# Performance work log

Hardware: AMD Instinct MI355X
Metric: run time of the kernel (lower is better)

## Reference

```python
import jax, jax.numpy as jnp
import numpy as np
from jax import lax

BOS, EOS = 1, 2
MAX_LEN = 16
BEAM = 4
VOCAB = 32000
INF = 1e9


def _gather_beams(x, idx):
    # x: [B, K, ...] or [B, K]; idx: [B, k]
    if x.ndim == 3:
        return jnp.take_along_axis(x, idx[:, :, None], axis=1)
    return jnp.take_along_axis(x, idx, axis=1)


def setup_inputs() -> dict:
    key = jax.random.key(0)
    k1, k2, k3, k4 = jax.random.split(key, 4)
    B, S, D = 16, 128, 512
    return {
        "src_input": jax.random.randint(k1, (B, S), 0, VOCAB),
        "E_src": jax.random.normal(k2, (VOCAB, D), jnp.float32) * 0.02,
        "E_tgt": jax.random.normal(k3, (VOCAB, D), jnp.float32) * 0.02,
        "W": jax.random.normal(k4, (D, VOCAB), jnp.float32) * 0.02,
        "b": jnp.zeros((VOCAB,), jnp.float32),
    }


def _beam_search(src_input, E_src, E_tgt, W, b):
    B = src_input.shape[0]
    # tile_by_beam: repeat each batch row beam_size times
    src = jnp.repeat(src_input, BEAM, axis=0)                     # [B*BEAM, S]
    # stub encoder: embedding + masked mean pool (pad token = 0)
    enc = E_src[src]                                              # [B*BEAM, S, D]
    keep = (src != 0).astype(enc.dtype)[..., None]
    pooled = (enc * keep).sum(1) / jnp.maximum(keep.sum(1), 1.0)  # [B*BEAM, D]

    alive_seq = jnp.zeros((B, BEAM, MAX_LEN), jnp.int32).at[:, :, 0].set(BOS)
    alive_lp = jnp.full((B, BEAM), -jnp.inf, jnp.float32).at[:, 0].set(0.0)
    fin_seq = jnp.zeros((B, BEAM, MAX_LEN), jnp.int32)
    fin_scores = jnp.full((B, BEAM), -INF, jnp.float32)
    fin_flags = jnp.zeros((B, BEAM), bool)
    batch_fin = jnp.zeros((B,), bool)
    batch_idx = jnp.arange(B)[:, None]

    for t in range(MAX_LEN - 1):
        # stub decoder: last-token embedding + encoder summary -> vocab logits
        last = alive_seq[:, :, t].reshape(B * BEAM)
        logits = (E_tgt[last] + pooled) @ W + b                   # [B*BEAM, V]
        lp = jax.nn.log_softmax(logits, axis=-1).reshape(B, BEAM, VOCAB)
        log_probs = alive_lp[:, :, None] + lp                     # [B, BEAM, V]
        lpen = jnp.float32(t + 1)
        flat = (log_probs / lpen).reshape(B, BEAM * VOCAB)
        topk_scores, topk_ids = lax.top_k(flat, BEAM * 2)         # [B, 2*BEAM]
        topk_lp = topk_scores * lpen
        if t == 0:
            beam_idx = jnp.tile(jnp.arange(BEAM), (B, 2))
        else:
            beam_idx = topk_ids // VOCAB
        tok = topk_ids % VOCAB
        topk_seq = alive_seq[batch_idx, beam_idx]                 # [B, 2*BEAM, L]
        topk_seq = topk_seq.at[:, :, t + 1].set(tok.astype(jnp.int32))
        topk_fin = tok == EOS
        # alive set: penalize finished candidates
        curr = topk_scores + topk_fin.astype(jnp.float32) * -INF
        _, a_idx = lax.top_k(curr, BEAM)
        alive_seq = _gather_beams(topk_seq, a_idx)
        alive_lp = _gather_beams(topk_lp, a_idx)
        # finished set: penalize unfinished + already-finished batches
        fs = (topk_scores + (1.0 - topk_fin.astype(jnp.float32)) * -INF
              + batch_fin[:, None].astype(jnp.float32) * -INF)
        cand_seq = jnp.concatenate([fin_seq, topk_seq], axis=1)   # [B, 3*BEAM, L]
        cand_sc = jnp.concatenate([fin_scores, fs], axis=1)
        cand_fl = jnp.concatenate([fin_flags, topk_fin], axis=1)
        _, f_idx = lax.top_k(cand_sc, BEAM)
        fin_seq = _gather_beams(cand_seq, f_idx)
        fin_scores = _gather_beams(cand_sc, f_idx)
        fin_flags = _gather_beams(cand_fl, f_idx)
        # batch-finished lower-bound test
        lb_alive = alive_lp[:, 0] / lpen
        lowest_fin = jnp.min(fin_scores * fin_flags.astype(jnp.float32), axis=1)
        lowest_fin = lowest_fin + (1.0 - jnp.all(fin_flags, axis=1).astype(jnp.float32)) * -INF
        batch_fin = batch_fin | (lowest_fin >= lb_alive)
    return fin_seq, fin_scores


def reference(src_input, E_src, E_tgt, W, b):
    fin_seq, _ = _beam_search(src_input, E_src, E_tgt, W, b)
    return fin_seq[:, 0]  # one_best_output [B, MAX_LEN] int32
```

## Files before the change

### kernel.cpp

```cpp
#include <hip/hip_runtime.h>
#include <math.h>

#define BATCH 16
#define SRCLEN 128
#define DIM 512
#define VOCABSZ 32000
#define BEAM 4
#define MAXLEN 16
#define NROWS (BATCH*BEAM)
#define BOS_TOK 1
#define EOS_TOK 2
#define NEGINF 1e9f
#define CHUNKS 8
#define CHUNK 4000
#define PCH 8
#define PCL (SRCLEN/PCH)

__global__ __launch_bounds__(512) void k_pool2(const int* __restrict__ src,
                                               const float* __restrict__ Esrc,
                                               float* __restrict__ pp, float* __restrict__ pcnt) {
    int b = blockIdx.x, c = blockIdx.y;
    int d = threadIdx.x;
    float acc = 0.f, cnt = 0.f;
#pragma unroll
    for (int s = 0; s < PCL; ++s) {
        int tok = src[b * SRCLEN + c * PCL + s];
        if (tok != 0) { acc += Esrc[(size_t)tok * DIM + d]; cnt += 1.f; }
    }
    pp[(b * PCH + c) * DIM + d] = acc;
    if (d == 0) pcnt[b * PCH + c] = cnt;
}

__global__ __launch_bounds__(512) void k_poolred(const float* __restrict__ pp,
                                                 const float* __restrict__ pcnt,
                                                 float* __restrict__ pooled) {
    int b = blockIdx.x;
    int d = threadIdx.x;
    float acc = 0.f, cnt = 0.f;
#pragma unroll
    for (int c = 0; c < PCH; ++c) { acc += pp[(b * PCH + c) * DIM + d]; cnt += pcnt[b * PCH + c]; }
    pooled[b * DIM + d] = acc / fmaxf(cnt, 1.f);
}

__global__ __launch_bounds__(1024) void k_init(int* __restrict__ alive_seq, float* __restrict__ alive_lp,
                                               int* __restrict__ fin_seq, float* __restrict__ fin_scores,
                                               int* __restrict__ fin_flags, int* __restrict__ batch_fin) {
    int tid = threadIdx.x;
    alive_seq[tid] = (tid % MAXLEN == 0) ? BOS_TOK : 0;
    fin_seq[tid] = 0;
    if (tid < NROWS) {
        alive_lp[tid] = (tid % BEAM == 0) ? 0.f : -INFINITY;
        fin_scores[tid] = -NEGINF;
        fin_flags[tid] = 0;
    }
    if (tid < BATCH) batch_fin[tid] = 0;
}

__global__ __launch_bounds__(512) void k_x(const float* __restrict__ Etgt,
                                           const float* __restrict__ pooled,
                                           const int* __restrict__ alive_seq, int t,
                                           float* __restrict__ xT) {
    int i = blockIdx.x;
    int d = threadIdx.x;
    int last = alive_seq[i * MAXLEN + t];
    float v = Etgt[(size_t)last * DIM + d] + pooled[(i >> 2) * DIM + d];
    xT[d * NROWS + i] = v;
}

template<int DLEN>
__global__ __launch_bounds__(256) void k_gemm4(const float* __restrict__ xT,
                                               const float* __restrict__ W,
                                               float* __restrict__ partial) {
    int v  = blockIdx.x * 64 + (threadIdx.x & 63);
    int rq = __builtin_amdgcn_readfirstlane(threadIdx.x >> 6);
    int r0 = rq * 16;
    int z  = blockIdx.z;
    int d0 = z * DLEN;
    float acc[16];
#pragma unroll
    for (int i = 0; i < 16; ++i) acc[i] = 0.f;
    const float* wp = W + (size_t)d0 * VOCABSZ + v;
    const float* xp = xT + (size_t)d0 * NROWS + r0;
    for (int dd = 0; dd < DLEN; dd += 4) {
        float w0 = wp[0];
        float w1 = wp[(size_t)VOCABSZ];
        float w2 = wp[(size_t)2 * VOCABSZ];
        float w3 = wp[(size_t)3 * VOCABSZ];
        wp += (size_t)4 * VOCABSZ;
        const float* x0 = xp;
        const float* x1 = xp + NROWS;
        const float* x2 = xp + 2 * NROWS;
        const float* x3 = xp + 3 * NROWS;
        xp += 4 * NROWS;
#pragma unroll
        for (int i = 0; i < 16; ++i) acc[i] = fmaf(x0[i], w0, acc[i]);
#pragma unroll
        for (int i = 0; i < 16; ++i) acc[i] = fmaf(x1[i], w1, acc[i]);
#pragma unroll
        for (int i = 0; i < 16; ++i) acc[i] = fmaf(x2[i], w2, acc[i]);
#pragma unroll
        for (int i = 0; i < 16; ++i) acc[i] = fmaf(x3[i], w3, acc[i]);
    }
    float* op = partial + (size_t)z * NROWS * VOCABSZ + (size_t)r0 * VOCABSZ + v;
#pragma unroll
    for (int i = 0; i < 16; ++i) op[(size_t)i * VOCABSZ] = acc[i];
}

template<int NZ>
__global__ __launch_bounds__(256) void k_part(const float* __restrict__ partial,
                                              const float* __restrict__ bias,
                                              float* __restrict__ pm, float* __restrict__ ps,
                                              float* __restrict__ ptopv, int* __restrict__ ptopi) {
    int row = blockIdx.x, ch = blockIdx.y;
    int tid = threadIdx.x;
    const size_t slab = (size_t)NROWS * VOCABSZ;
    const float4* lr4[NZ];
#pragma unroll
    for (int zz = 0; zz < NZ; ++zz)
        lr4[zz] = (const float4*)(partial + slab * zz + (size_t)row * VOCABSZ + ch * CHUNK);
    const float4* b4 = (const float4*)(bias + ch * CHUNK);

    float va[16]; int np = 0;
    float lv[8]; int li[8];
#pragma unroll
    for (int j = 0; j < 8; ++j) { lv[j] = -INFINITY; li[j] = 0x7FFFFFFF; }

#pragma unroll
    for (int j = 0; j < 4; ++j) {
        int idx = j * 256 + tid;
        if (idx < CHUNK / 4) {
            float4 q = lr4[0][idx];
#pragma unroll
            for (int zz = 1; zz < NZ; ++zz) {
                float4 q2 = lr4[zz][idx];
                q.x += q2.x; q.y += q2.y; q.z += q2.z; q.w += q2.w;
            }
            float4 bb = b4[idx];
            q.x += bb.x; q.y += bb.y; q.z += bb.z; q.w += bb.w;
            int gi = ch * CHUNK + idx * 4;
            float vals[4] = {q.x, q.y, q.z, q.w};
#pragma unroll
            for (int c = 0; c < 4; ++c) {
                float x = vals[c];
                va[np++] = x;
                int v = gi + c;
                if (x > lv[7] || (x == lv[7] && v < li[7])) {
                    lv[7] = x; li[7] = v;
#pragma unroll
                    for (int q2 = 7; q2 > 0; --q2) {
                        bool sw = (lv[q2] > lv[q2-1]) || (lv[q2] == lv[q2-1] && li[q2] < li[q2-1]);
                        if (sw) { float tv = lv[q2]; lv[q2] = lv[q2-1]; lv[q2-1] = tv;
                                  int  ti = li[q2]; li[q2] = li[q2-1]; li[q2-1] = ti; }
                    }
                }
            }
        }
    }

    __shared__ float sred[256];
    float m_t = -INFINITY;
    for (int j = 0; j < np; ++j) m_t = fmaxf(m_t, va[j]);
    sred[tid] = m_t;
    __syncthreads();
    for (int s = 128; s > 0; s >>= 1) { if (tid < s) sred[tid] = fmaxf(sred[tid], sred[tid+s]); __syncthreads(); }
    float m = sred[0];
    __syncthreads();

    float se = 0.f;
    for (int j = 0; j < np; ++j) se += expf(va[j] - m);
    sred[tid] = se;
    __syncthreads();
    for (int s = 128; s > 0; s >>= 1) { if (tid < s) sred[tid] += sred[tid+s]; __syncthreads(); }
    if (tid == 0) { pm[row * CHUNKS + ch] = m; ps[row * CHUNKS + ch] = sred[0]; }

    __shared__ unsigned long long skey[256];
    int pos = 0;
    float* otv = ptopv + ((size_t)row * CHUNKS + ch) * 8;
    int*   oti = ptopi + ((size_t)row * CHUNKS + ch) * 8;
    for (int r = 0; r < 8; ++r) {
        unsigned long long mykey = 0ULL;
        if (pos < 8) {
            unsigned int fb = __float_as_uint(lv[pos]);
            fb = fb ^ ((fb >> 31) ? 0xFFFFFFFFu : 0x80000000u);
            mykey = ((unsigned long long)fb << 32) | (unsigned long long)(0xFFFFFFFFu - (unsigned int)li[pos]);
        }
        skey[tid] = mykey;
        __syncthreads();
        for (int s = 128; s > 0; s >>= 1) { if (tid < s) skey[tid] = (skey[tid] > skey[tid+s]) ? skey[tid] : skey[tid+s]; __syncthreads(); }
        unsigned long long best = skey[0];
        __syncthreads();
        if (mykey == best && mykey != 0ULL) {
            otv[r] = lv[pos];
            oti[r] = li[pos];
            pos++;
        }
        __syncthreads();
    }
}

__device__ inline unsigned long long packkey(float v, int idx) {
    unsigned int fb = __float_as_uint(v);
    fb = fb ^ ((fb >> 31) ? 0xFFFFFFFFu : 0x80000000u);
    return ((unsigned long long)fb << 32) | (unsigned long long)(0xFFFFFFFFu - (unsigned int)idx);
}
__device__ inline float unpack_val(unsigned long long k) {
    unsigned int fb = (unsigned int)(k >> 32);
    fb = fb ^ ((fb >> 31) ? 0x80000000u : 0xFFFFFFFFu);
    return __uint_as_float(fb);
}
__device__ inline int unpack_id(unsigned long long k) {
    return (int)(0xFFFFFFFFu - (unsigned int)(k & 0xFFFFFFFFu));
}
__device__ inline unsigned long long shflxor64(unsigned long long x, int mask) {
    unsigned int lo = (unsigned int)x, hi = (unsigned int)(x >> 32);
    lo = (unsigned int)__shfl_xor((int)lo, mask, 64);
    hi = (unsigned int)__shfl_xor((int)hi, mask, 64);
    return ((unsigned long long)hi << 32) | (unsigned long long)lo;
}
__device__ inline unsigned long long wavemax64(unsigned long long k) {
#pragma unroll
    for (int off = 1; off < 64; off <<= 1) {
        unsigned long long o = shflxor64(k, off);
        k = (o > k) ? o : k;
    }
    return k;
}

__global__ __launch_bounds__(64) void k_mergesel(const float* __restrict__ pm, const float* __restrict__ ps,
                                                 const float* __restrict__ ptopv, const int* __restrict__ ptopi,
                                                 int* __restrict__ alive_seq, float* __restrict__ alive_lp,
                                                 int* __restrict__ fin_seq, float* __restrict__ fin_scores,
                                                 int* __restrict__ fin_flags, int* __restrict__ batch_fin, int t) {
    int b = blockIdx.x;
    int tid = threadIdx.x;
    __shared__ int aseq_old[BEAM][MAXLEN]; __shared__ int fseq_old[BEAM][MAXLEN];
    __shared__ float s_tlp[8]; __shared__ int s_ttok[8], s_tbeam[8];
    __shared__ int s_aidx[4], s_fidx[4];
    __shared__ float s_nfsc[4]; __shared__ int s_nffl[4];
    float lpen = (float)(t + 1);

    { int k = tid >> 4, p = tid & 15;
      aseq_old[k][p] = alive_seq[(b * BEAM + k) * MAXLEN + p];
      fseq_old[k][p] = fin_seq[(b * BEAM + k) * MAXLEN + p]; }

    float rv[4]; int ri[4];
#pragma unroll
    for (int k = 0; k < 4; ++k) {
        rv[k] = ptopv[(size_t)(b * BEAM + k) * 64 + tid];
        ri[k] = ptopi[(size_t)(b * BEAM + k) * 64 + tid];
    }

    float alp[4], fsc[4]; int ffl[4];
#pragma unroll
    for (int k = 0; k < 4; ++k) {
        alp[k] = alive_lp[b * BEAM + k];
        fsc[k] = fin_scores[b * BEAM + k];
        ffl[k] = fin_flags[b * BEAM + k];
    }
    int bf_old = batch_fin[b];

    float srm[4], srl[4];
#pragma unroll
    for (int k = 0; k < 4; ++k) {
        float m = -INFINITY;
#pragma unroll
        for (int c = 0; c < CHUNKS; ++c) m = fmaxf(m, pm[(b * BEAM + k) * CHUNKS + c]);
        float s = 0.f;
#pragma unroll
        for (int c = 0; c < CHUNKS; ++c) s += ps[(b * BEAM + k) * CHUNKS + c] * expf(pm[(b * BEAM + k) * CHUNKS + c] - m);
        srm[k] = m; srl[k] = logf(s);
    }

    unsigned long long key[4];
#pragma unroll
    for (int k = 0; k < 4; ++k) {
        float sh = rv[k] - srm[k];
        float lp = sh - srl[k];
        float full = alp[k] + lp;
        float cv = full / lpen;
        key[k] = packkey(cv, k * VOCABSZ + ri[k]);
    }
    {
        unsigned long long tmp;
#define CSW(a,b) if (key[b] > key[a]) { tmp = key[a]; key[a] = key[b]; key[b] = tmp; }
        CSW(0,1) CSW(2,3) CSW(0,2) CSW(1,3) CSW(1,2)
#undef CSW
    }

    float tscore[8], tlp[8]; int ttok[8], tbeam[8], tfin[8];
    int pos = 0;
#pragma unroll
    for (int r = 0; r < 8; ++r) {
        unsigned long long head = (pos == 0) ? key[0] : (pos == 1) ? key[1] :
                                  (pos == 2) ? key[2] : (pos == 3) ? key[3] : 0ULL;
        unsigned long long mx = wavemax64(head);
        if (head == mx && head != 0ULL) pos++;
        float sc = unpack_val(mx);
        int id = unpack_id(mx);
        tscore[r] = sc;
        tlp[r] = sc * lpen;
        ttok[r] = id % VOCABSZ;
        tbeam[r] = id / VOCABSZ;
        tfin[r] = (ttok[r] == EOS_TOK) ? 1 : 0;
    }

    int aidx[4];
    {
        float curr[8];
#pragma unroll
        for (int j = 0; j < 8; ++j) curr[j] = tscore[j] + (tfin[j] ? -NEGINF : 0.0f);
        unsigned int used = 0;
#pragma unroll
        for (int r = 0; r < 4; ++r) {
            float bv = 0.f; int bj = -1;
#pragma unroll
            for (int j = 0; j < 8; ++j) {
                bool skip = (used >> j) & 1u;
                bool better = !skip && (bj < 0 || curr[j] > bv);
                if (better) { bv = curr[j]; bj = j; }
            }
            used |= 1u << bj; aidx[r] = bj;
        }
    }
    int fidx[4]; float nfsc[4]; int nffl[4];
    {
        float fscand[12]; int fflcand[12];
#pragma unroll
        for (int j = 0; j < 4; ++j) { fscand[j] = fsc[j]; fflcand[j] = ffl[j]; }
#pragma unroll
        for (int q = 0; q < 8; ++q) {
            float t1 = tscore[q] + (tfin[q] ? 0.0f : -NEGINF);
            float t2 = t1 + (bf_old ? -NEGINF : 0.0f);
            fscand[4 + q] = t2; fflcand[4 + q] = tfin[q];
        }
        unsigned int used = 0;
#pragma unroll
        for (int r = 0; r < 4; ++r) {
            float bv = 0.f; int bj = -1;
#pragma unroll
            for (int j = 0; j < 12; ++j) {
                bool skip = (used >> j) & 1u;
                bool better = !skip && (bj < 0 || fscand[j] > bv);
                if (better) { bv = fscand[j]; bj = j; }
            }
            used |= 1u << bj; fidx[r] = bj;
            nfsc[r] = bv;
        }
#pragma unroll
        for (int r = 0; r < 4; ++r) {
            int bj = fidx[r]; int fl = 0;
#pragma unroll
            for (int j = 0; j < 12; ++j) if (bj == j) fl = fflcand[j];
            nffl[r] = fl;
        }
    }

    if (tid == 0) {
#pragma unroll
        for (int r = 0; r < 8; ++r) { s_tlp[r] = tlp[r]; s_ttok[r] = ttok[r]; s_tbeam[r] = tbeam[r]; }
#pragma unroll
        for (int r = 0; r < 4; ++r) { s_aidx[r] = aidx[r]; s_fidx[r] = fidx[r]; s_nfsc[r] = nfsc[r]; s_nffl[r] = nffl[r]; }
    }
    __syncthreads();

    { int k = tid >> 4, p = tid & 15;
      int j = s_aidx[k];
      int val = (p == t + 1) ? s_ttok[j] : aseq_old[s_tbeam[j]][p];
      alive_seq[(b * BEAM + k) * MAXLEN + p] = val;
      int fi = s_fidx[k]; int fval;
      if (fi < 4) fval = fseq_old[fi][p];
      else { int q = fi - 4; fval = (p == t + 1) ? s_ttok[q] : aseq_old[s_tbeam[q]][p]; }
      fin_seq[(b * BEAM + k) * MAXLEN + p] = fval; }

    if (tid < 4) {
        alive_lp[b * BEAM + tid] = s_tlp[s_aidx[tid]];
        fin_scores[b * BEAM + tid] = s_nfsc[tid];
        fin_flags[b * BEAM + tid] = s_nffl[tid];
    }
    if (tid == 0) {
        float lb = s_tlp[s_aidx[0]] / lpen;
        float lowest = nfsc[0] * (nffl[0] ? 1.f : 0.f);
        int allf = nffl[0];
#pragma unroll
        for (int k2 = 1; k2 < 4; ++k2) {
            float pz = nfsc[k2] * (nffl[k2] ? 1.f : 0.f);
            lowest = fminf(lowest, pz);
            allf = allf && nffl[k2];
        }
        lowest = lowest + (allf ? 0.f : -NEGINF);
        batch_fin[b] = bf_old || (lowest >= lb);
    }
}

__global__ __launch_bounds__(256) void k_out(const int* __restrict__ fin_seq, float* __restrict__ out) {
    int tid = threadIdx.x;
    if (tid < BATCH * MAXLEN) {
        int b = tid / MAXLEN, p = tid % MAXLEN;
        out[tid] = (float)fin_seq[(b * BEAM + 0) * MAXLEN + p];
    }
}

extern "C" void kernel_launch(void* const* d_in, const int* in_sizes, int n_in,
                              void* d_out, int out_size, void* d_ws, size_t ws_size,
                              hipStream_t stream) {
    const int*   src  = (const int*)d_in[0];
    const float* Esrc = (const float*)d_in[1];
    const float* Etgt = (const float*)d_in[2];
    const float* W    = (const float*)d_in[3];
    const float* bias = (const float*)d_in[4];
    float* out = (float*)d_out;

    const size_t slab = (size_t)NROWS * VOCABSZ * 4;
    const bool big = ws_size >= 4 * slab + (1u << 20);
    const int NZ = big ? 4 : 1;

    char* p = (char*)d_ws;
    float* partial    = (float*)p; p += NZ * slab;
    float* pooled     = (float*)p; p += BATCH * DIM * 4;
    float* xT         = (float*)p; p += DIM * NROWS * 4;
    float* pp         = (float*)p; p += BATCH * PCH * DIM * 4;
    float* pcnt       = (float*)p; p += BATCH * PCH * 4;
    float* pm         = (float*)p; p += NROWS * CHUNKS * 4;
    float* ps         = (float*)p; p += NROWS * CHUNKS * 4;
    float* ptopv      = (float*)p; p += NROWS * CHUNKS * 8 * 4;
    int*   ptopi      = (int*)p;   p += NROWS * CHUNKS * 8 * 4;
    int*   alive_seq  = (int*)p;   p += NROWS * MAXLEN * 4;
    int*   fin_seq    = (int*)p;   p += NROWS * MAXLEN * 4;
    float* alive_lp   = (float*)p; p += NROWS * 4;
    float* fin_scores = (float*)p; p += NROWS * 4;
    int*   fin_flags  = (int*)p;   p += NROWS * 4;
    int*   batch_fin  = (int*)p;   p += BATCH * 4;

    k_pool2<<<dim3(BATCH, PCH), DIM, 0, stream>>>(src, Esrc, pp, pcnt);
    k_poolred<<<BATCH, DIM, 0, stream>>>(pp, pcnt, pooled);
    k_init<<<1, 1024, 0, stream>>>(alive_seq, alive_lp, fin_seq, fin_scores, fin_flags, batch_fin);
    for (int t = 0; t < MAXLEN - 1; ++t) {
        k_x<<<NROWS, DIM, 0, stream>>>(Etgt, pooled, alive_seq, t, xT);
        if (big) {
            k_gemm4<DIM/4><<<dim3(VOCABSZ / 64, 1, 4), 256, 0, stream>>>(xT, W, partial);
            k_part<4><<<dim3(NROWS, CHUNKS), 256, 0, stream>>>(partial, bias, pm, ps, ptopv, ptopi);
        } else {
            k_gemm4<DIM><<<dim3(VOCABSZ / 64, 1, 1), 256, 0, stream>>>(xT, W, partial);
            k_part<1><<<dim3(NROWS, CHUNKS), 256, 0, stream>>>(partial, bias, pm, ps, ptopv, ptopi);
        }
        k_mergesel<<<BATCH, 64, 0, stream>>>(pm, ps, ptopv, ptopi, alive_seq, alive_lp,
                                             fin_seq, fin_scores, fin_flags, batch_fin, t);
    }
    k_out<<<1, 256, 0, stream>>>(fin_seq, out);
}
```

Before: 1.284 ms.

## Rewrite per-chunk softmax/top-k with 1024-thread blocks and wave-shuffle reductions

The partial-logit reduction kernel now launches 1024 threads per chunk, so each thread handles one float4 instead of looping over four. Max and sum-exp are computed with wavefront shuffle reductions plus a small shared array, replacing tree reductions over shared memory that needed a barrier at every step. The per-thread insertion-sorted top-8 is replaced by a 4-element sorting network followed by eight wave-wide argmax rounds per wavefront and a final 64-lane merge. This removes the 8 rounds of shared-memory tree reduction, each with many barriers, that the old top-k selection used. The cost is larger blocks, which may limit occupancy, and more 64-bit shuffles.

```diff
diff --git a/kernel.cpp b/kernel.cpp
--- a/kernel.cpp
+++ b/kernel.cpp
@@ -16,6 +16,34 @@
 #define PCH 8
 #define PCL (SRCLEN/PCH)
 
+__device__ inline unsigned long long packkey(float v, int idx) {
+    unsigned int fb = __float_as_uint(v);
+    fb = fb ^ ((fb >> 31) ? 0xFFFFFFFFu : 0x80000000u);
+    return ((unsigned long long)fb << 32) | (unsigned long long)(0xFFFFFFFFu - (unsigned int)idx);
+}
+__device__ inline float unpack_val(unsigned long long k) {
+    unsigned int fb = (unsigned int)(k >> 32);
+    fb = fb ^ ((fb >> 31) ? 0x80000000u : 0xFFFFFFFFu);
+    return __uint_as_float(fb);
+}
+__device__ inline int unpack_id(unsigned long long k) {
+    return (int)(0xFFFFFFFFu - (unsigned int)(k & 0xFFFFFFFFu));
+}
+__device__ inline unsigned long long shflxor64(unsigned long long x, int mask) {
+    unsigned int lo = (unsigned int)x, hi = (unsigned int)(x >> 32);
+    lo = (unsigned int)__shfl_xor((int)lo, mask, 64);
+    hi = (unsigned int)__shfl_xor((int)hi, mask, 64);
+    return ((unsigned long long)hi << 32) | (unsigned long long)lo;
+}
+__device__ inline unsigned long long wavemax64(unsigned long long k) {
+#pragma unroll
+    for (int off = 1; off < 64; off <<= 1) {
+        unsigned long long o = shflxor64(k, off);
+        k = (o > k) ? o : k;
+    }
+    return k;
+}
+
 __global__ __launch_bounds__(512) void k_pool2(const int* __restrict__ src,
                                                const float* __restrict__ Esrc,
                                                float* __restrict__ pp, float* __restrict__ pcnt) {
@@ -107,123 +135,107 @@
 }
 
 template<int NZ>
-__global__ __launch_bounds__(256) void k_part(const float* __restrict__ partial,
-                                              const float* __restrict__ bias,
-                                              float* __restrict__ pm, float* __restrict__ ps,
-                                              float* __restrict__ ptopv, int* __restrict__ ptopi) {
+__global__ __launch_bounds__(1024) void k_part(const float* __restrict__ partial,
+                                               const float* __restrict__ bias,
+                                               float* __restrict__ pm, float* __restrict__ ps,
+                                               float* __restrict__ ptopv, int* __restrict__ ptopi) {
     int row = blockIdx.x, ch = blockIdx.y;
     int tid = threadIdx.x;
+    int lane = tid & 63;
+    int wv = tid >> 6;
     const size_t slab = (size_t)NROWS * VOCABSZ;
-    const float4* lr4[NZ];
-#pragma unroll
-    for (int zz = 0; zz < NZ; ++zz)
-        lr4[zz] = (const float4*)(partial + slab * zz + (size_t)row * VOCABSZ + ch * CHUNK);
-    const float4* b4 = (const float4*)(bias + ch * CHUNK);
-
-    float va[16]; int np = 0;
-    float lv[8]; int li[8];
-#pragma unroll
-    for (int j = 0; j < 8; ++j) { lv[j] = -INFINITY; li[j] = 0x7FFFFFFF; }
-
-#pragma unroll
-    for (int j = 0; j < 4; ++j) {
-        int idx = j * 256 + tid;
-        if (idx < CHUNK / 4) {
-            float4 q = lr4[0][idx];
-#pragma unroll
-            for (int zz = 1; zz < NZ; ++zz) {
-                float4 q2 = lr4[zz][idx];
-                q.x += q2.x; q.y += q2.y; q.z += q2.z; q.w += q2.w;
-            }
-            float4 bb = b4[idx];
-            q.x += bb.x; q.y += bb.y; q.z += bb.z; q.w += bb.w;
-            int gi = ch * CHUNK + idx * 4;
-            float vals[4] = {q.x, q.y, q.z, q.w};
-#pragma unroll
-            for (int c = 0; c < 4; ++c) {
-                float x = vals[c];
-                va[np++] = x;
-                int v = gi + c;
-                if (x > lv[7] || (x == lv[7] && v < li[7])) {
-                    lv[7] = x; li[7] = v;
-#pragma unroll
-                    for (int q2 = 7; q2 > 0; --q2) {
-                        bool sw = (lv[q2] > lv[q2-1]) || (lv[q2] == lv[q2-1] && li[q2] < li[q2-1]);
-                        if (sw) { float tv = lv[q2]; lv[q2] = lv[q2-1]; lv[q2-1] = tv;
-                                  int  ti = li[q2]; li[q2] = li[q2-1]; li[q2-1] = ti; }
-                    }
-                }
-            }
-        }
-    }
-
-    __shared__ float sred[256];
-    float m_t = -INFINITY;
-    for (int j = 0; j < np; ++j) m_t = fmaxf(m_t, va[j]);
-    sred[tid] = m_t;
+    const bool valid = tid < (CHUNK / 4);
+
+    float vals[4] = {-INFINITY, -INFINITY, -INFINITY, -INFINITY};
+    if (valid) {
+        const float4* l0 = (const float4*)(partial + (size_t)row * VOCABSZ + ch * CHUNK);
+        float4 q = l0[tid];
+#pragma unroll
+        for (int zz = 1; zz < NZ; ++zz) {
+            const float4* lz = (const float4*)(partial + slab * zz + (size_t)row * VOCABSZ + ch * CHUNK);
+            float4 q2 = lz[tid];
+            q.x += q2.x; q.y += q2.y; q.z += q2.z; q.w += q2.w;
+        }
+        float4 bb = ((const float4*)(bias + ch * CHUNK))[tid];
+        vals[0] = q.x + bb.x; vals[1] = q.y + bb.y; vals[2] = q.z + bb.z; vals[3] = q.w + bb.w;
+    }
+
+    float m_t = fmaxf(fmaxf(vals[0], vals[1]), fmaxf(vals[2], vals[3]));
+#pragma unroll
+    for (int off = 1; off < 64; off <<= 1) m_t = fmaxf(m_t, __shfl_xor(m_t, off, 64));
+    __shared__ float swred[16];
+    if (lane == 0) swred[wv] = m_t;
     __syncthreads();
-    for (int s = 128; s > 0; s >>= 1) { if (tid < s) sred[tid] = fmaxf(sred[tid], sred[tid+s]); __syncthreads(); }
-    float m = sred[0];
+    float m = swred[0];
+#pragma unroll
+    for (int w = 1; w < 16; ++w) m = fmaxf(m, swred[w]);
     __syncthreads();
 
     float se = 0.f;
-    for (int j = 0; j < np; ++j) se += expf(va[j] - m);
-    sred[tid] = se;
+    if (valid) {
+#pragma unroll
+        for (int c = 0; c < 4; ++c) se += expf(vals[c] - m);
+    }
+#pragma unroll
+    for (int off = 1; off < 64; off <<= 1) se += __shfl_xor(se, off, 64);
+    if (lane == 0) swred[wv] = se;
     __syncthreads();
-    for (int s = 128; s > 0; s >>= 1) { if (tid < s) sred[tid] += sred[tid+s]; __syncthreads(); }
-    if (tid == 0) { pm[row * CHUNKS + ch] = m; ps[row * CHUNKS + ch] = sred[0]; }
-
-    __shared__ unsigned long long skey[256];
-    int pos = 0;
-    float* otv = ptopv + ((size_t)row * CHUNKS + ch) * 8;
-    int*   oti = ptopi + ((size_t)row * CHUNKS + ch) * 8;
-    for (int r = 0; r < 8; ++r) {
-        unsigned long long mykey = 0ULL;
-        if (pos < 8) {
-            unsigned int fb = __float_as_uint(lv[pos]);
-            fb = fb ^ ((fb >> 31) ? 0xFFFFFFFFu : 0x80000000u);
-            mykey = ((unsigned long long)fb << 32) | (unsigned long long)(0xFFFFFFFFu - (unsigned int)li[pos]);
-        }
-        skey[tid] = mykey;
-        __syncthreads();
-        for (int s = 128; s > 0; s >>= 1) { if (tid < s) skey[tid] = (skey[tid] > skey[tid+s]) ? skey[tid] : skey[tid+s]; __syncthreads(); }
-        unsigned long long best = skey[0];
-        __syncthreads();
-        if (mykey == best && mykey != 0ULL) {
-            otv[r] = lv[pos];
-            oti[r] = li[pos];
-            pos++;
-        }
-        __syncthreads();
-    }
-}
-
-__device__ inline unsigned long long packkey(float v, int idx) {
-    unsigned int fb = __float_as_uint(v);
-    fb = fb ^ ((fb >> 31) ? 0xFFFFFFFFu : 0x80000000u);
-    return ((unsigned long long)fb << 32) | (unsigned long long)(0xFFFFFFFFu - (unsigned int)idx);
-}
-__device__ inline float unpack_val(unsigned long long k) {
-    unsigned int fb = (unsigned int)(k >> 32);
-    fb = fb ^ ((fb >> 31) ? 0x80000000u : 0xFFFFFFFFu);
-    return __uint_as_float(fb);
-}
-__device__ inline int unpack_id(unsigned long long k) {
-    return (int)(0xFFFFFFFFu - (unsigned int)(k & 0xFFFFFFFFu));
-}
-__device__ inline unsigned long long shflxor64(unsigned long long x, int mask) {
-    unsigned int lo = (unsigned int)x, hi = (unsigned int)(x >> 32);
-    lo = (unsigned int)__shfl_xor((int)lo, mask, 64);
-    hi = (unsigned int)__shfl_xor((int)hi, mask, 64);
-    return ((unsigned long long)hi << 32) | (unsigned long long)lo;
-}
-__device__ inline unsigned long long wavemax64(unsigned long long k) {
-#pragma unroll
-    for (int off = 1; off < 64; off <<= 1) {
-        unsigned long long o = shflxor64(k, off);
-        k = (o > k) ? o : k;
-    }
-    return k;
+    if (tid == 0) {
+        float s = 0.f;
+#pragma unroll
+        for (int w = 0; w < 16; ++w) s += swred[w];
+        pm[row * CHUNKS + ch] = m;
+        ps[row * CHUNKS + ch] = s;
+    }
+
+    int gi = ch * CHUNK + tid * 4;
+    unsigned long long k0 = 0ULL, k1 = 0ULL, k2 = 0ULL, k3 = 0ULL;
+    if (valid) {
+        k0 = packkey(vals[0], gi);
+        k1 = packkey(vals[1], gi + 1);
+        k2 = packkey(vals[2], gi + 2);
+        k3 = packkey(vals[3], gi + 3);
+    }
+    {
+        unsigned long long tswp;
+#define CSW(a,b) if (b > a) { tswp = a; a = b; b = tswp; }
+        CSW(k0,k1) CSW(k2,k3) CSW(k0,k2) CSW(k1,k3) CSW(k1,k2)
+#undef CSW
+    }
+    __shared__ unsigned long long skey[128];
+    {
+        int pos = 0;
+        unsigned long long wtop[8];
+#pragma unroll
+        for (int r = 0; r < 8; ++r) {
+            unsigned long long head = (pos == 0) ? k0 : (pos == 1) ? k1 :
+                                      (pos == 2) ? k2 : (pos == 3) ? k3 : 0ULL;
+            unsigned long long mx = wavemax64(head);
+            if (head == mx && head != 0ULL) pos++;
+            wtop[r] = mx;
+        }
+        if (lane == 0) {
+#pragma unroll
+            for (int r = 0; r < 8; ++r) skey[wv * 8 + r] = wtop[r];
+        }
+    }
+    __syncthreads();
+    if (tid < 64) {
+        unsigned long long a = skey[tid];
+        unsigned long long b2 = skey[64 + tid];
+        unsigned long long hi = (a > b2) ? a : b2;
+        unsigned long long lo = (a > b2) ? b2 : a;
+        float* otv = ptopv + ((size_t)row * CHUNKS + ch) * 8;
+        int*   oti = ptopi + ((size_t)row * CHUNKS + ch) * 8;
+        int pos = 0;
+#pragma unroll
+        for (int r = 0; r < 8; ++r) {
+            unsigned long long head = (pos == 0) ? hi : (pos == 1) ? lo : 0ULL;
+            unsigned long long mx = wavemax64(head);
+            if (head == mx && head != 0ULL) pos++;
+            if (tid == 0) { otv[r] = unpack_val(mx); oti[r] = unpack_id(mx); }
+        }
+    }
 }
 
 __global__ __launch_bounds__(64) void k_mergesel(const float* __restrict__ pm, const float* __restrict__ ps,
@@ -438,10 +450,10 @@
         k_x<<<NROWS, DIM, 0, stream>>>(Etgt, pooled, alive_seq, t, xT);
         if (big) {
             k_gemm4<DIM/4><<<dim3(VOCABSZ / 64, 1, 4), 256, 0, stream>>>(xT, W, partial);
-            k_part<4><<<dim3(NROWS, CHUNKS), 256, 0, stream>>>(partial, bias, pm, ps, ptopv, ptopi);
+            k_part<4><<<dim3(NROWS, CHUNKS), 1024, 0, stream>>>(partial, bias, pm, ps, ptopv, ptopi);
         } else {
             k_gemm4<DIM><<<dim3(VOCABSZ / 64, 1, 1), 256, 0, stream>>>(xT, W, partial);
-            k_part<1><<<dim3(NROWS, CHUNKS), 256, 0, stream>>>(partial, bias, pm, ps, ptopv, ptopi);
+            k_part<1><<<dim3(NROWS, CHUNKS), 1024, 0, stream>>>(partial, bias, pm, ps, ptopv, ptopi);
         }
         k_mergesel<<<BATCH, 64, 0, stream>>>(pm, ps, ptopv, ptopi, alive_seq, alive_lp,
                                              fin_seq, fin_scores, fin_flags, batch_fin, t);
```

Result: faster. 1.122 ms (-12.6%).
